# Optimization experiments

Hardware: AMD Instinct MI355X
Metric: run time of the kernel (lower is better)

Reference implementation:

```python
import jax, jax.numpy as jnp
import numpy as np

F = 18      # n_frames (hard-coded by norm_scale vectors in the original)
P = 1024    # n_partitions
E = 2048    # n_hidden == n_features
H = 8       # n_head
HD = E // H
C = 64      # n_cluster


def setup_inputs() -> dict:
    key = jax.random.key(0)
    ks = jax.random.split(key, 11)
    s = 0.02
    return {
        "emb": jax.random.normal(ks[0], (F, P, E), jnp.float32),
        "Wq": jax.random.normal(ks[1], (E, E), jnp.float32) * s,
        "Wk": jax.random.normal(ks[2], (E, E), jnp.float32) * s,
        "Wv": jax.random.normal(ks[3], (E, E), jnp.float32) * s,
        "bq": jax.random.normal(ks[4], (E,), jnp.float32) * s,
        "bk": jax.random.normal(ks[5], (E,), jnp.float32) * s,
        "bv": jax.random.normal(ks[6], (E,), jnp.float32) * s,
        "Wo": jax.random.normal(ks[7], (E, E), jnp.float32) * s,
        "bo": jax.random.normal(ks[8], (E,), jnp.float32) * s,
        "Wmp": jax.random.normal(ks[9], (C, E), jnp.float32) * s,
        "bmp": jax.random.normal(ks[10], (C,), jnp.float32) * s,
    }


def reference(emb, Wq, Wk, Wv, bq, bk, bv, Wo, bo, Wmp, bmp):
    # message_passing path of CRF_SelfAttention (eval mode, dropout off).
    # The original folds each window's frames into the batch dim
    # (cat(chunk(group2, scale, 0), 1)), so MultiheadAttention runs with
    # sequence length 1: each token attends only to itself.
    x = emb.reshape(F * P, E)                        # tokens
    q = (x @ Wq.T + bq).reshape(-1, H, HD)
    k = (x @ Wk.T + bk).reshape(-1, H, HD)
    v = (x @ Wv.T + bv).reshape(-1, H, HD)
    scores = jnp.einsum('nhd,nhd->nh', q, k) / jnp.sqrt(jnp.float32(HD))
    attn = jax.nn.softmax(scores[..., None], axis=-1)  # [N,H,1] -> all ones
    ctx = attn * v                                     # [N,H,HD]
    Y = (ctx.reshape(-1, E) @ Wo.T + bo).reshape(F, P, E)

    # Per scale, frame t is covered by counts_s[t] identical window outputs
    # (the hard-coded norm_scale vectors); accumulate then divide.
    # NOTE: the original uses multihead_attn_scale2 for ALL scales.
    t = jnp.arange(F)
    gaccum = jnp.zeros_like(Y)
    for scale in (2, 4, 6):
        counts = jnp.minimum(jnp.minimum(t + 1, scale),
                             jnp.minimum(F - t, F - scale + 1)).astype(Y.dtype)
        gval = Y * counts[:, None, None]
        gaccum = gaccum + gval / counts[:, None, None]
    pairwise = 0.25 * gaccum                          # [F,P,E]
    pairwise = pairwise.transpose(1, 0, 2)            # [P,F,E]
    return pairwise @ Wmp.T + bmp                     # [P,F,C]
```

## Files before the change

kernel.cpp:

```cpp
#include <hip/hip_runtime.h>
#include <hip/hip_bf16.h>
#include <stdint.h>

typedef __bf16 bf16_t;
typedef __bf16 bf16x8 __attribute__((ext_vector_type(8)));
typedef float f32x4 __attribute__((ext_vector_type(4)));

#define Edim 2048
#define Cdim 64
#define Fdim 18
#define Pdim 1024
#define Ntok (Fdim * Pdim)

__device__ __forceinline__ bf16x8 cvt8(const float* __restrict__ p) {
    float4 lo = *(const float4*)p;
    float4 hi = *(const float4*)(p + 4);
    bf16x8 r;
    r[0] = (bf16_t)lo.x; r[1] = (bf16_t)lo.y; r[2] = (bf16_t)lo.z; r[3] = (bf16_t)lo.w;
    r[4] = (bf16_t)hi.x; r[5] = (bf16_t)hi.y; r[6] = (bf16_t)hi.z; r[7] = (bf16_t)hi.w;
    return r;
}

__global__ __launch_bounds__(256) void splitk_gemm_kernel(
    const float* __restrict__ Am, const float* __restrict__ Bm,
    float* __restrict__ outAcc)
{
    const int tid  = threadIdx.x;
    const int wave = tid >> 6;
    const int lane = tid & 63;
    const int l15  = lane & 15;
    const int koct = lane >> 4;
    const int n0   = blockIdx.x * 64;
    const int kb   = blockIdx.y * 256;

    f32x4 acc[4] = {};

    for (int k0 = kb; k0 < kb + 256; k0 += 32) {
        bf16x8 a = cvt8(Am + (size_t)(wave * 16 + l15) * Edim + k0 + koct * 8);
        #pragma unroll
        for (int t = 0; t < 4; ++t) {
            const float* src = Bm + (size_t)(k0 + koct * 8) * Edim + n0 + t * 16 + l15;
            bf16x8 b;
            #pragma unroll
            for (int j = 0; j < 8; ++j) b[j] = (bf16_t)src[(size_t)j * Edim];
            acc[t] = __builtin_amdgcn_mfma_f32_16x16x32_bf16(a, b, acc[t], 0, 0, 0);
        }
    }

    #pragma unroll
    for (int t = 0; t < 4; ++t) {
        #pragma unroll
        for (int r = 0; r < 4; ++r) {
            int m = wave * 16 + koct * 4 + r;
            int n = n0 + t * 16 + l15;
            atomicAdd(&outAcc[(size_t)m * Edim + n], acc[t][r]);
        }
    }
}

__global__ __launch_bounds__(256) void matvec_kernel(
    const float* __restrict__ Wo, const float* __restrict__ bv,
    const float* __restrict__ bo, float* __restrict__ u)
{
    const int tid  = threadIdx.x;
    const int wave = tid >> 6;
    const int lane = tid & 63;
    const int r    = blockIdx.x * 4 + wave;

    const float* wp = Wo + (size_t)r * Edim;
    float s = 0.f;
    #pragma unroll
    for (int c = 0; c < 8; ++c) {
        float4 w4 = *(const float4*)(wp + c * 256 + lane * 4);
        float4 b4 = *(const float4*)(bv + c * 256 + lane * 4);
        s += w4.x * b4.x + w4.y * b4.y + w4.z * b4.z + w4.w * b4.w;
    }
    #pragma unroll
    for (int off = 32; off > 0; off >>= 1) s += __shfl_down(s, off);
    if (lane == 0) u[r] = s + bo[r];
}

__global__ __launch_bounds__(256) void bias2_kernel(
    const float* __restrict__ Wmp, const float* __restrict__ u,
    const float* __restrict__ bmp, float* __restrict__ b_eff)
{
    const int c   = blockIdx.x;
    const int tid = threadIdx.x;

    const float* wp = Wmp + (size_t)c * Edim + tid * 8;
    const float* up = u + tid * 8;
    float s = 0.f;
    #pragma unroll
    for (int j = 0; j < 8; ++j) s += wp[j] * up[j];

    #pragma unroll
    for (int off = 32; off > 0; off >>= 1) s += __shfl_down(s, off);

    __shared__ float red[4];
    if ((tid & 63) == 0) red[tid >> 6] = s;
    __syncthreads();
    if (tid == 0)
        b_eff[c] = 0.75f * (red[0] + red[1] + red[2] + red[3]) + bmp[c];
}

__global__ __launch_bounds__(256) void convert_kernel(
    const float* __restrict__ Wf, bf16_t* __restrict__ Wb)
{
    const int i = (blockIdx.x * 256 + threadIdx.x) * 8;
    float4 lo = *(const float4*)(Wf + i);
    float4 hi = *(const float4*)(Wf + i + 4);
    bf16x8 r;
    r[0] = (bf16_t)(0.75f * lo.x); r[1] = (bf16_t)(0.75f * lo.y);
    r[2] = (bf16_t)(0.75f * lo.z); r[3] = (bf16_t)(0.75f * lo.w);
    r[4] = (bf16_t)(0.75f * hi.x); r[5] = (bf16_t)(0.75f * hi.y);
    r[6] = (bf16_t)(0.75f * hi.z); r[7] = (bf16_t)(0.75f * hi.w);
    *(bf16x8*)(Wb + i) = r;
}

__global__ __launch_bounds__(256) void main_gemm_kernel(
    const float* __restrict__ X, const bf16_t* __restrict__ Weff,
    const float* __restrict__ b_eff, float* __restrict__ out)
{
    __shared__ float red[3 * 64 * 17];

    const int tid  = threadIdx.x;
    const int wave = tid >> 6;
    const int lane = tid & 63;
    const int l15  = lane & 15;
    const int koct = lane >> 4;

    const int rowa = blockIdx.x * 16 + l15;
    const float* xp = X + (size_t)rowa * Edim;
    const int kbase = wave * 512;

    f32x4 acc[4] = {};

    #pragma unroll 2
    for (int k0 = kbase; k0 < kbase + 512; k0 += 32) {
        bf16x8 a = cvt8(xp + k0 + koct * 8);
        #pragma unroll
        for (int t = 0; t < 4; ++t) {
            bf16x8 b = *(const bf16x8*)(Weff + (size_t)(t * 16 + l15) * Edim + k0 + koct * 8);
            acc[t] = __builtin_amdgcn_mfma_f32_16x16x32_bf16(a, b, acc[t], 0, 0, 0);
        }
    }

    if (wave != 0) {
        float* dst = &red[(wave - 1) * 1088 + lane * 17];
        #pragma unroll
        for (int t = 0; t < 4; ++t)
            #pragma unroll
            for (int r = 0; r < 4; ++r) dst[t * 4 + r] = acc[t][r];
    }
    __syncthreads();
    if (wave == 0) {
        #pragma unroll
        for (int w = 0; w < 3; ++w) {
            const float* srcp = &red[w * 1088 + lane * 17];
            #pragma unroll
            for (int t = 0; t < 4; ++t)
                #pragma unroll
                for (int r = 0; r < 4; ++r) acc[t][r] += srcp[t * 4 + r];
        }
        const int mbase = blockIdx.x * 16 + koct * 4;
        #pragma unroll
        for (int t = 0; t < 4; ++t) {
            const int c  = t * 16 + l15;
            const float be = b_eff[c];
            #pragma unroll
            for (int r = 0; r < 4; ++r) {
                const int m = mbase + r;
                const int f = m >> 10;
                const int p = m & 1023;
                out[(size_t)(p * Fdim + f) * Cdim + c] = acc[t][r] + be;
            }
        }
    }
}

extern "C" void kernel_launch(void* const* d_in, const int* in_sizes, int n_in,
                              void* d_out, int out_size, void* d_ws, size_t ws_size,
                              hipStream_t stream)
{
    const float* emb = (const float*)d_in[0];
    const float* Wv  = (const float*)d_in[3];
    const float* bv  = (const float*)d_in[6];
    const float* Wo  = (const float*)d_in[7];
    const float* bo  = (const float*)d_in[8];
    const float* Wmp = (const float*)d_in[9];
    const float* bmp = (const float*)d_in[10];

    float*  A_f32 = (float*)d_ws;
    float*  W_f32 = A_f32 + (size_t)Cdim * Edim;
    bf16_t* Weffb = (bf16_t*)(W_f32 + (size_t)Cdim * Edim);
    float*  u     = (float*)(Weffb + (size_t)Cdim * Edim);
    float*  beff  = u + Edim;

    float* out = (float*)d_out;

    hipMemsetAsync(A_f32, 0, (size_t)Cdim * Edim * sizeof(float), stream);
    hipMemsetAsync(W_f32, 0, (size_t)Cdim * Edim * sizeof(float), stream);

    splitk_gemm_kernel<<<dim3(32, 8), 256, 0, stream>>>(Wmp, Wo, A_f32);
    matvec_kernel<<<512, 256, 0, stream>>>(Wo, bv, bo, u);
    splitk_gemm_kernel<<<dim3(32, 8), 256, 0, stream>>>(A_f32, Wv, W_f32);
    convert_kernel<<<64, 256, 0, stream>>>(W_f32, Weffb);
    bias2_kernel<<<64, 256, 0, stream>>>(Wmp, u, bmp, beff);
    main_gemm_kernel<<<Ntok / 16, 256, 0, stream>>>(emb, Weffb, beff, out);
}
```

Before: 308.3 us.

## Replace atomic split-K with partial buffers and double main GEMM row tile

The weight-folding split-K GEMMs now write per-split partial results to workspace buffers instead of using atomicAdd. Separate reduce kernels sum the partials and convert them to bf16, which drops the memsets and the convert kernel, and the split count rises to 16. The main GEMM now processes 32 rows per block with two accumulator sets, so each loaded Weff fragment is reused twice, at the cost of more registers and larger shared memory. The intermediate A matrix is also stored as bf16, adding a second rounding step.

After: 296.5 us. 3.8% less time.

```diff
diff --git a/kernel.cpp b/kernel.cpp
--- a/kernel.cpp
+++ b/kernel.cpp
@@ -4,6 +4,7 @@
 
 typedef __bf16 bf16_t;
 typedef __bf16 bf16x8 __attribute__((ext_vector_type(8)));
+typedef __bf16 bf16x4 __attribute__((ext_vector_type(4)));
 typedef float f32x4 __attribute__((ext_vector_type(4)));
 
 #define Edim 2048
@@ -11,6 +12,7 @@
 #define Fdim 18
 #define Pdim 1024
 #define Ntok (Fdim * Pdim)
+#define KSPLIT 16
 
 __device__ __forceinline__ bf16x8 cvt8(const float* __restrict__ p) {
     float4 lo = *(const float4*)p;
@@ -21,9 +23,10 @@
     return r;
 }
 
+template <bool A_IS_F32>
 __global__ __launch_bounds__(256) void splitk_gemm_kernel(
-    const float* __restrict__ Am, const float* __restrict__ Bm,
-    float* __restrict__ outAcc)
+    const void* __restrict__ Am, const float* __restrict__ Bm,
+    float* __restrict__ parts)
 {
     const int tid  = threadIdx.x;
     const int wave = tid >> 6;
@@ -31,12 +34,18 @@
     const int l15  = lane & 15;
     const int koct = lane >> 4;
     const int n0   = blockIdx.x * 64;
-    const int kb   = blockIdx.y * 256;
+    const int kb   = blockIdx.y * 128;
 
     f32x4 acc[4] = {};
 
-    for (int k0 = kb; k0 < kb + 256; k0 += 32) {
-        bf16x8 a = cvt8(Am + (size_t)(wave * 16 + l15) * Edim + k0 + koct * 8);
+    #pragma unroll
+    for (int i = 0; i < 4; ++i) {
+        const int k0 = kb + i * 32;
+        bf16x8 a;
+        if constexpr (A_IS_F32)
+            a = cvt8((const float*)Am + (size_t)(wave * 16 + l15) * Edim + k0 + koct * 8);
+        else
+            a = *(const bf16x8*)((const bf16_t*)Am + (size_t)(wave * 16 + l15) * Edim + k0 + koct * 8);
         #pragma unroll
         for (int t = 0; t < 4; ++t) {
             const float* src = Bm + (size_t)(k0 + koct * 8) * Edim + n0 + t * 16 + l15;
@@ -47,15 +56,32 @@
         }
     }
 
+    float* dst = parts + (size_t)blockIdx.y * (Cdim * Edim);
     #pragma unroll
     for (int t = 0; t < 4; ++t) {
         #pragma unroll
         for (int r = 0; r < 4; ++r) {
             int m = wave * 16 + koct * 4 + r;
             int n = n0 + t * 16 + l15;
-            atomicAdd(&outAcc[(size_t)m * Edim + n], acc[t][r]);
-        }
-    }
+            dst[(size_t)m * Edim + n] = acc[t][r];
+        }
+    }
+}
+
+__global__ __launch_bounds__(256) void reduce_parts_kernel(
+    const float* __restrict__ parts, bf16_t* __restrict__ out, float scale)
+{
+    const int idx = (blockIdx.x * 256 + threadIdx.x) * 4;
+    float4 s = {0.f, 0.f, 0.f, 0.f};
+    #pragma unroll
+    for (int j = 0; j < KSPLIT; ++j) {
+        float4 v = *(const float4*)(parts + (size_t)j * (Cdim * Edim) + idx);
+        s.x += v.x; s.y += v.y; s.z += v.z; s.w += v.w;
+    }
+    bf16x4 r;
+    r[0] = (bf16_t)(scale * s.x); r[1] = (bf16_t)(scale * s.y);
+    r[2] = (bf16_t)(scale * s.z); r[3] = (bf16_t)(scale * s.w);
+    *(bf16x4*)(out + idx) = r;
 }
 
 __global__ __launch_bounds__(256) void matvec_kernel(
@@ -103,25 +129,11 @@
         b_eff[c] = 0.75f * (red[0] + red[1] + red[2] + red[3]) + bmp[c];
 }
 
-__global__ __launch_bounds__(256) void convert_kernel(
-    const float* __restrict__ Wf, bf16_t* __restrict__ Wb)
-{
-    const int i = (blockIdx.x * 256 + threadIdx.x) * 8;
-    float4 lo = *(const float4*)(Wf + i);
-    float4 hi = *(const float4*)(Wf + i + 4);
-    bf16x8 r;
-    r[0] = (bf16_t)(0.75f * lo.x); r[1] = (bf16_t)(0.75f * lo.y);
-    r[2] = (bf16_t)(0.75f * lo.z); r[3] = (bf16_t)(0.75f * lo.w);
-    r[4] = (bf16_t)(0.75f * hi.x); r[5] = (bf16_t)(0.75f * hi.y);
-    r[6] = (bf16_t)(0.75f * hi.z); r[7] = (bf16_t)(0.75f * hi.w);
-    *(bf16x8*)(Wb + i) = r;
-}
-
 __global__ __launch_bounds__(256) void main_gemm_kernel(
     const float* __restrict__ X, const bf16_t* __restrict__ Weff,
     const float* __restrict__ b_eff, float* __restrict__ out)
 {
-    __shared__ float red[3 * 64 * 17];
+    __shared__ float red[3 * 64 * 33];
 
     const int tid  = threadIdx.x;
     const int wave = tid >> 6;
@@ -129,50 +141,60 @@
     const int l15  = lane & 15;
     const int koct = lane >> 4;
 
-    const int rowa = blockIdx.x * 16 + l15;
-    const float* xp = X + (size_t)rowa * Edim;
+    const int rbase = blockIdx.x * 32;
+    const float* x0 = X + (size_t)(rbase + l15) * Edim;
+    const float* x1 = x0 + (size_t)16 * Edim;
     const int kbase = wave * 512;
 
-    f32x4 acc[4] = {};
-
-    #pragma unroll 2
+    f32x4 acc[2][4] = {};
+
+    #pragma unroll 4
     for (int k0 = kbase; k0 < kbase + 512; k0 += 32) {
-        bf16x8 a = cvt8(xp + k0 + koct * 8);
+        bf16x8 a0 = cvt8(x0 + k0 + koct * 8);
+        bf16x8 a1 = cvt8(x1 + k0 + koct * 8);
         #pragma unroll
         for (int t = 0; t < 4; ++t) {
             bf16x8 b = *(const bf16x8*)(Weff + (size_t)(t * 16 + l15) * Edim + k0 + koct * 8);
-            acc[t] = __builtin_amdgcn_mfma_f32_16x16x32_bf16(a, b, acc[t], 0, 0, 0);
+            acc[0][t] = __builtin_amdgcn_mfma_f32_16x16x32_bf16(a0, b, acc[0][t], 0, 0, 0);
+            acc[1][t] = __builtin_amdgcn_mfma_f32_16x16x32_bf16(a1, b, acc[1][t], 0, 0, 0);
         }
     }
 
     if (wave != 0) {
-        float* dst = &red[(wave - 1) * 1088 + lane * 17];
-        #pragma unroll
-        for (int t = 0; t < 4; ++t)
-            #pragma unroll
-            for (int r = 0; r < 4; ++r) dst[t * 4 + r] = acc[t][r];
+        float* dst = &red[(wave - 1) * 2112 + lane * 33];
+        #pragma unroll
+        for (int e = 0; e < 2; ++e)
+            #pragma unroll
+            for (int t = 0; t < 4; ++t)
+                #pragma unroll
+                for (int r = 0; r < 4; ++r) dst[e * 16 + t * 4 + r] = acc[e][t][r];
     }
     __syncthreads();
     if (wave == 0) {
         #pragma unroll
         for (int w = 0; w < 3; ++w) {
-            const float* srcp = &red[w * 1088 + lane * 17];
-            #pragma unroll
-            for (int t = 0; t < 4; ++t)
+            const float* srcp = &red[w * 2112 + lane * 33];
+            #pragma unroll
+            for (int e = 0; e < 2; ++e)
                 #pragma unroll
-                for (int r = 0; r < 4; ++r) acc[t][r] += srcp[t * 4 + r];
-        }
-        const int mbase = blockIdx.x * 16 + koct * 4;
-        #pragma unroll
-        for (int t = 0; t < 4; ++t) {
-            const int c  = t * 16 + l15;
-            const float be = b_eff[c];
-            #pragma unroll
-            for (int r = 0; r < 4; ++r) {
-                const int m = mbase + r;
-                const int f = m >> 10;
-                const int p = m & 1023;
-                out[(size_t)(p * Fdim + f) * Cdim + c] = acc[t][r] + be;
+                for (int t = 0; t < 4; ++t)
+                    #pragma unroll
+                    for (int r = 0; r < 4; ++r) acc[e][t][r] += srcp[e * 16 + t * 4 + r];
+        }
+        #pragma unroll
+        for (int e = 0; e < 2; ++e) {
+            const int mbase = rbase + e * 16 + koct * 4;
+            #pragma unroll
+            for (int t = 0; t < 4; ++t) {
+                const int c  = t * 16 + l15;
+                const float be = b_eff[c];
+                #pragma unroll
+                for (int r = 0; r < 4; ++r) {
+                    const int m = mbase + r;
+                    const int f = m >> 10;
+                    const int p = m & 1023;
+                    out[(size_t)(p * Fdim + f) * Cdim + c] = acc[e][t][r] + be;
+                }
             }
         }
     }
@@ -190,21 +212,21 @@
     const float* Wmp = (const float*)d_in[9];
     const float* bmp = (const float*)d_in[10];
 
-    float*  A_f32 = (float*)d_ws;
-    float*  W_f32 = A_f32 + (size_t)Cdim * Edim;
-    bf16_t* Weffb = (bf16_t*)(W_f32 + (size_t)Cdim * Edim);
-    float*  u     = (float*)(Weffb + (size_t)Cdim * Edim);
-    float*  beff  = u + Edim;
+    const size_t PART = (size_t)Cdim * Edim;
+    float*  parts1 = (float*)d_ws;
+    float*  parts2 = parts1 + (size_t)KSPLIT * PART;
+    bf16_t* A_bf   = (bf16_t*)(parts2 + (size_t)KSPLIT * PART);
+    bf16_t* Weffb  = A_bf + PART;
+    float*  u      = (float*)(Weffb + PART);
+    float*  beff   = u + Edim;
 
     float* out = (float*)d_out;
 
-    hipMemsetAsync(A_f32, 0, (size_t)Cdim * Edim * sizeof(float), stream);
-    hipMemsetAsync(W_f32, 0, (size_t)Cdim * Edim * sizeof(float), stream);
-
-    splitk_gemm_kernel<<<dim3(32, 8), 256, 0, stream>>>(Wmp, Wo, A_f32);
     matvec_kernel<<<512, 256, 0, stream>>>(Wo, bv, bo, u);
-    splitk_gemm_kernel<<<dim3(32, 8), 256, 0, stream>>>(A_f32, Wv, W_f32);
-    convert_kernel<<<64, 256, 0, stream>>>(W_f32, Weffb);
     bias2_kernel<<<64, 256, 0, stream>>>(Wmp, u, bmp, beff);
-    main_gemm_kernel<<<Ntok / 16, 256, 0, stream>>>(emb, Weffb, beff, out);
-}
+    splitk_gemm_kernel<true><<<dim3(32, KSPLIT), 256, 0, stream>>>(Wmp, Wo, parts1);
+    reduce_parts_kernel<<<128, 256, 0, stream>>>(parts1, A_bf, 1.0f);
+    splitk_gemm_kernel<false><<<dim3(32, KSPLIT), 256, 0, stream>>>(A_bf, Wv, parts2);
+    reduce_parts_kernel<<<128, 256, 0, stream>>>(parts2, Weffb, 0.75f);
+    main_gemm_kernel<<<Ntok / 32, 256, 0, stream>>>(emb, Weffb, beff, out);
+}
```
